# Optimization experiments

Measured on AMD Instinct MI355X. Metric: run time of the kernel, lower is better.

Reference implementation:

```python
import jax, jax.numpy as jnp
import numpy as np

T, B = 128, 64
STATE_DIM, LATENT_DIM, AC_DIM, MS_DIM = 32, 16, 8, 8
STATE_EMBED, AC_EMBED, HIDDEN, OUT_DIM = 64, 16, 64, 18


def setup_inputs() -> dict:
    key = jax.random.key(0)
    ks = jax.random.split(key, 18)
    f = lambda i, shape: jax.random.normal(ks[i], shape, jnp.float32)
    s = 0.05  # param scale
    return dict(
        state=f(0, (T, B, STATE_DIM)),
        latent_mean=f(1, (T, B, LATENT_DIM)),
        latent_logvar=f(2, (T, B, LATENT_DIM)) * 0.1,
        latent_mean_t=f(3, (T, B, LATENT_DIM)),
        latent_logvar_t=f(4, (T, B, LATENT_DIM)) * 0.1,
        agent_character=f(5, (T, B, AC_DIM)),
        mental_state=f(6, (T, B, MS_DIM)),
        partner_actions=jax.random.randint(ks[7], (T, B), 0, OUT_DIM, jnp.int32),
        dones=(jax.random.uniform(ks[8], (T, B)) < 0.05).astype(jnp.float32),
        W_state=f(9, (STATE_DIM, STATE_EMBED)) * s, b_state=jnp.zeros(STATE_EMBED),
        W_ac=f(10, (AC_DIM, AC_EMBED)) * s, b_ac=jnp.zeros(AC_EMBED),
        W_embed=f(11, (STATE_EMBED + AC_EMBED, HIDDEN)) * s, b_embed=jnp.zeros(HIDDEN),
        W_hid=f(12, (AC_EMBED + MS_DIM, HIDDEN)) * s, b_hid=jnp.zeros(HIDDEN),
        Wi=f(13, (HIDDEN, 3 * HIDDEN)) * s, bi=jnp.zeros(3 * HIDDEN),
        Wh_rz=f(14, (HIDDEN, 2 * HIDDEN)) * s,
        Wh_n=f(15, (HIDDEN, HIDDEN)) * s, bh_n=jnp.zeros(HIDDEN),
        W_out=f(16, (HIDDEN, OUT_DIM)) * s, b_out=jnp.zeros(OUT_DIM),
    )


def reference(state, latent_mean, latent_logvar, latent_mean_t, latent_logvar_t,
              agent_character, mental_state, partner_actions, dones,
              W_state, b_state, W_ac, b_ac, W_embed, b_embed, W_hid, b_hid,
              Wi, bi, Wh_rz, Wh_n, bh_n, W_out, b_out):
    Tn = state.shape[0]
    # ---- KL between consecutive latent Gaussians (with N(0,I) prior at t=0) ----
    lm = jnp.concatenate((latent_mean, latent_mean_t), -1)      # (T,B,2L)
    lv = jnp.concatenate((latent_logvar, latent_logvar_t), -1)
    G = lm.shape[-1]
    am = jnp.concatenate((jnp.zeros((1,) + lm.shape[1:], lm.dtype), lm))
    al = jnp.concatenate((jnp.zeros((1,) + lv.shape[1:], lv.dtype), lv))
    mu, m = am[1:], am[:-1]
    logE, logS = al[1:], al[:-1]
    kl = 0.5 * (logS.sum(-1) - logE.sum(-1) - G
                + jnp.exp(logE - logS).sum(-1)
                + ((m - mu) ** 2 / jnp.exp(logS)).sum(-1))      # (T,B)
    kl_loss = kl.sum()
    # ---- feature extractors ----
    se = jax.nn.relu(state @ W_state + b_state)                 # (T,B,SE)
    ae = jax.nn.relu(agent_character @ W_ac + b_ac)             # (T,B,AE)
    embed = jnp.concatenate((se, ae), -1) @ W_embed + b_embed   # (T,B,H)
    hidden = jnp.concatenate((ae, mental_state), -1) @ W_hid + b_hid  # (T,B,H)
    # ---- k-batch: K=T shifted trajectories, zero-padded at the tail ----
    idx = jnp.arange(Tn)[:, None] + jnp.arange(Tn)[None, :]     # (K,T)
    valid = idx < Tn                                            # (K,T) bool
    cidx = jnp.minimum(idx, Tn - 1)
    vf = valid.astype(embed.dtype)[..., None]                   # (K,T,1)
    k_embed = embed[cidx] * vf[..., None]                       # (K,T,B,H)
    k_hidden = hidden[cidx] * vf[..., None]                     # (K,T,B,H)
    k_dones = dones[cidx] * vf                                  # (K,T,B)
    k_actions = jnp.where(valid[..., None], partner_actions[cidx], 0)  # (K,T,B)
    # fill_to_first_true: 1 up to and including the first done of each k-traj
    episode_mask = (jnp.cumsum(k_dones, axis=1) - k_dones == 0).astype(embed.dtype)  # (K,T,B)
    # ---- GRU scan over timestep axis, vectorized over (K,B) ----
    h0 = k_hidden[:, 0]                                         # (K,B,H)
    xs = (jnp.moveaxis(k_embed, 1, 0), jnp.moveaxis(k_hidden, 1, 0), jnp.moveaxis(k_dones, 1, 0))

    def step(h, x):
        x_t, h0_t, d_t = x                                      # (K,B,H),(K,B,H),(K,B)
        h = jnp.where(d_t[..., None] > 0, h0_t, h)              # reset on done
        ir, iz, i_n = jnp.split(x_t @ Wi + bi, 3, -1)
        hr, hz = jnp.split(h @ Wh_rz, 2, -1)
        r = jax.nn.sigmoid(ir + hr)
        z = jax.nn.sigmoid(iz + hz)
        n = jnp.tanh(i_n + r * (h @ Wh_n + bh_n))
        h_new = (1.0 - z) * n + z * h
        return h_new, h_new

    _, hs = jax.lax.scan(step, h0, xs)                          # (T,K,B,H)
    logp = jax.nn.log_softmax(hs @ W_out + b_out, -1)           # (T,K,B,O)
    k_act_t = jnp.moveaxis(k_actions, 1, 0)                     # (T,K,B)
    nll = -jnp.take_along_axis(logp, k_act_t[..., None], -1)[..., 0]  # (T,K,B)
    mask = valid.T[:, :, None].astype(nll.dtype) * jnp.moveaxis(episode_mask, 1, 0)
    recon_loss = (nll * mask).sum(axis=1)                       # sum over K -> (T,B)
    return kl_loss, recon_loss
```

## Files before the change

### kernel.cpp

```cpp
#include <hip/hip_runtime.h>


#define XH_OFF   0
#define AUX_OFF  4194304
#define CTR_OFF  4227072

typedef float f32x16 __attribute__((ext_vector_type(16)));
typedef _Float16 h2 __attribute__((ext_vector_type(2)));

#if __has_builtin(__builtin_amdgcn_fdot2)
#define DOT2(a, b, c) __builtin_amdgcn_fdot2((a), (b), (c), false)
#else
#define DOT2(a, b, c) ((c) + (float)(a).x * (float)(b).x + (float)(a).y * (float)(b).y)
#endif

__device__ __forceinline__ h2 pack_pair(float h) {
  int hb = __builtin_bit_cast(int, h);
  int hp = __builtin_amdgcn_mov_dpp(hb, 0xB1, 0xF, 0xF, true);
  return __builtin_bit_cast(h2, __builtin_amdgcn_cvt_pkrtz(h, __builtin_bit_cast(float, hp)));
}

__device__ __forceinline__ float row16_scan_add(float v) {
  int t;
  t = __builtin_amdgcn_update_dpp(0, __builtin_bit_cast(int, v), 0x111, 0xF, 0xF, true);
  v += __builtin_bit_cast(float, t);
  t = __builtin_amdgcn_update_dpp(0, __builtin_bit_cast(int, v), 0x112, 0xF, 0xF, true);
  v += __builtin_bit_cast(float, t);
  t = __builtin_amdgcn_update_dpp(0, __builtin_bit_cast(int, v), 0x114, 0xF, 0xF, true);
  v += __builtin_bit_cast(float, t);
  t = __builtin_amdgcn_update_dpp(0, __builtin_bit_cast(int, v), 0x118, 0xF, 0xF, true);
  v += __builtin_bit_cast(float, t);
  return v;
}

__global__ __launch_bounds__(256, 1) void precompute_kernel(
    const float* __restrict__ state, const float* __restrict__ ac, const float* __restrict__ ms,
    const float* __restrict__ Wst, const float* __restrict__ bst,
    const float* __restrict__ Wac, const float* __restrict__ bac,
    const float* __restrict__ Wem, const float* __restrict__ bem,
    const float* __restrict__ Whd, const float* __restrict__ bhd,
    const float* __restrict__ Wi,  const float* __restrict__ bi,
    const float* __restrict__ lm, const float* __restrict__ lv,
    const float* __restrict__ lmt, const float* __restrict__ lvt,
    const float* __restrict__ dones, const int* __restrict__ actions,
    _Float16* __restrict__ xh, int* __restrict__ aux, float* __restrict__ out) {
  __shared__ float sWst[32 * 64];
  __shared__ float sWem[80 * 64];
  __shared__ float sWhd[24 * 64];
  __shared__ float sWac[8 * 16];
  __shared__ float sb[208];
  __shared__ float sin_[4][48];
  __shared__ float sse[4][80];
  __shared__ float semb[4][64];
  __shared__ float ps[4];
  int tid = threadIdx.x, lane = tid & 63, w = tid >> 6;

  if (blockIdx.x >= 256) {
    float total = 0.f;
    for (int it = 0; it < 16; ++it) {
      int idx = ((int)blockIdx.x - 256) * 256 + tid + it * 16384;
      int g = idx & 31;
      int pair = idx >> 5;
      const float* M = (g < 16) ? lm : lmt;
      const float* V = (g < 16) ? lv : lvt;
      int cur = pair * 16 + (g & 15);
      float mu = M[cur], lE = V[cur];
      float m = 0.f, lS = 0.f;
      if (pair >= 64) { m = M[cur - 1024]; lS = V[cur - 1024]; }
      float d = m - mu;
      total += 0.5f * (lS - lE - 1.f + __expf(lE - lS) + d * d * __expf(-lS));
    }
    #pragma unroll
    for (int off = 32; off; off >>= 1) total += __shfl_xor(total, off);
    if (lane == 0) ps[w] = total;
    __syncthreads();
    if (tid == 0) atomicAdd(out, ps[0] + ps[1] + ps[2] + ps[3]);
    return;
  }

  f32x16 wi0[4], wi1[4], wi2[4];
  #pragma unroll
  for (int k = 0; k < 64; ++k) {
    wi0[k >> 4][k & 15] = Wi[k * 192 + lane];
    wi1[k >> 4][k & 15] = Wi[k * 192 + 64 + lane];
    wi2[k >> 4][k & 15] = Wi[k * 192 + 128 + lane];
  }
  for (int i = tid; i < 32 * 64; i += 256) sWst[i] = Wst[i];
  for (int i = tid; i < 80 * 64; i += 256) sWem[i] = Wem[i];
  for (int i = tid; i < 24 * 64; i += 256) sWhd[i] = Whd[i];
  for (int i = tid; i < 8 * 16; i += 256) sWac[i] = Wac[i];
  if (tid < 64) sb[tid] = bst[tid];
  if (tid < 16) sb[64 + tid] = bac[tid];
  if (tid < 64) sb[80 + tid] = bem[tid];
  if (tid < 64) sb[144 + tid] = bhd[tid];
  float bi0 = bi[lane], bi1 = bi[64 + lane], bi2 = bi[128 + lane];
  __syncthreads();
  for (int cnt = 0; cnt < 8; ++cnt) {
    int pair = blockIdx.x * 32 + w * 8 + cnt;
    if (lane < 32)      sin_[w][lane] = state[pair * 32 + lane];
    else if (lane < 40) sin_[w][lane] = ac[pair * 8 + (lane - 32)];
    else if (lane < 48) sin_[w][lane] = ms[pair * 8 + (lane - 40)];
    if (lane == 0) aux[pair] = (dones[pair] > 0.f ? (int)0x80000000 : 0) | actions[pair];
    __syncthreads();
    float se = sb[lane];
    #pragma unroll
    for (int k = 0; k < 32; ++k) se += sin_[w][k] * sWst[k * 64 + lane];
    se = fmaxf(se, 0.f);
    float ae = 0.f;
    if (lane < 16) {
      ae = sb[64 + lane];
      #pragma unroll
      for (int k = 0; k < 8; ++k) ae += sin_[w][32 + k] * sWac[k * 16 + lane];
      ae = fmaxf(ae, 0.f);
    }
    __syncthreads();
    sse[w][lane] = se;
    if (lane < 16) sse[w][64 + lane] = ae;
    __syncthreads();
    float em = sb[80 + lane];
    #pragma unroll
    for (int k = 0; k < 80; ++k) em += sse[w][k] * sWem[k * 64 + lane];
    float hd = sb[144 + lane];
    #pragma unroll
    for (int k = 0; k < 16; ++k) hd += sse[w][64 + k] * sWhd[k * 64 + lane];
    #pragma unroll
    for (int k = 0; k < 8; ++k) hd += sin_[w][40 + k] * sWhd[(16 + k) * 64 + lane];
    semb[w][lane] = em;
    __syncthreads();
    float x0 = bi0, x1 = bi1, x2 = bi2;
    #pragma unroll
    for (int k = 0; k < 64; ++k) {
      float e = semb[w][k];
      x0 += e * wi0[k >> 4][k & 15];
      x1 += e * wi1[k >> 4][k & 15];
      x2 += e * wi2[k >> 4][k & 15];
    }
    _Float16* xo = xh + pair * 256;
    xo[lane] = (_Float16)x0; xo[64 + lane] = (_Float16)x1;
    xo[128 + lane] = (_Float16)x2; xo[192 + lane] = (_Float16)hd;
    __syncthreads();
  }
}

__global__ __launch_bounds__(64, 2) void rollout_kernel(
    const _Float16* __restrict__ xh, const int* __restrict__ aux,
    const float* __restrict__ Whrz, const float* __restrict__ Whn,
    const float* __restrict__ bhn, const float* __restrict__ Wout,
    const float* __restrict__ bout, float* __restrict__ out,
    unsigned int* __restrict__ ctrs) {
  __shared__ __attribute__((aligned(16))) h2 sh2[32];
  int lane = threadIdx.x;
  int row = (lane < 18) ? lane : 0;
  h2 Wr[32], Wz[32], Wn[32], Wo[32];
  #pragma unroll
  for (int k = 0; k < 32; ++k) {
    Wr[k] = h2{(_Float16)Whrz[(2 * k) * 128 + lane],      (_Float16)Whrz[(2 * k + 1) * 128 + lane]};
    Wz[k] = h2{(_Float16)Whrz[(2 * k) * 128 + 64 + lane], (_Float16)Whrz[(2 * k + 1) * 128 + 64 + lane]};
    Wn[k] = h2{(_Float16)Whn[(2 * k) * 64 + lane],        (_Float16)Whn[(2 * k + 1) * 64 + lane]};
    Wo[k] = h2{(_Float16)Wout[(2 * k) * 18 + row],        (_Float16)Wout[(2 * k + 1) * 18 + row]};
  }
  float bhn_r = bhn[lane];
  float bo_r = bout[row];
  __syncthreads();
  const uint4* shv = (const uint4*)sh2;
  int q = blockIdx.x & 7;
  while (true) {
    int i = 0;
    if (lane == 0) i = (int)atomicAdd(&ctrs[q], 1u);
    i = __shfl(i, 0);
    if (i >= 1024) break;
    int t = i >> 3, b = ((i & 7) << 3) | q;
    int u = t;
    int pr = (t << 6) | b;
    const _Float16* xb = xh + pr * 256;
    float h = (float)xb[192 + lane];
    float x0 = (float)xb[lane], x1 = (float)xb[64 + lane], x2 = (float)xb[128 + lane];
    int ax = aux[pr];
    if ((lane & 1) == 0) sh2[lane >> 1] = pack_pair(h);
    for (int s = 0;; ++s) {
      int un = (u < 127) ? u + 1 : 127;
      int prn = (un << 6) | b;
      const _Float16* xn = xh + prn * 256;
      float nx0 = (float)xn[lane], nx1 = (float)xn[64 + lane], nx2 = (float)xn[128 + lane];
      float nh = (float)xn[192 + lane];
      int nax = aux[prn];
      float ara = x0, arb = 0.f, aza = x1, azb = 0.f, ana = 0.f, anb = 0.f;
      #pragma unroll
      for (int qq = 0; qq < 8; ++qq) {
        uint4 hv = shv[qq];
        h2 a0 = __builtin_bit_cast(h2, hv.x);
        h2 a1 = __builtin_bit_cast(h2, hv.y);
        h2 a2 = __builtin_bit_cast(h2, hv.z);
        h2 a3 = __builtin_bit_cast(h2, hv.w);
        ara = DOT2(a0, Wr[4 * qq + 0], ara); arb = DOT2(a1, Wr[4 * qq + 1], arb);
        ara = DOT2(a2, Wr[4 * qq + 2], ara); arb = DOT2(a3, Wr[4 * qq + 3], arb);
        aza = DOT2(a0, Wz[4 * qq + 0], aza); azb = DOT2(a1, Wz[4 * qq + 1], azb);
        aza = DOT2(a2, Wz[4 * qq + 2], aza); azb = DOT2(a3, Wz[4 * qq + 3], azb);
        ana = DOT2(a0, Wn[4 * qq + 0], ana); anb = DOT2(a1, Wn[4 * qq + 1], anb);
        ana = DOT2(a2, Wn[4 * qq + 2], ana); anb = DOT2(a3, Wn[4 * qq + 3], anb);
      }
      float ar = ara + arb, az = aza + azb, an = ana + anb;
      float r = __builtin_amdgcn_rcpf(1.f + __expf(-ar));
      float z = __builtin_amdgcn_rcpf(1.f + __expf(-az));
      float pre = x2 + r * (an + bhn_r);
      float n = 1.f - 2.f * __builtin_amdgcn_rcpf(1.f + __expf(2.f * pre));
      float hn = (1.f - z) * n + z * h;
      if ((lane & 1) == 0) sh2[lane >> 1] = pack_pair(hn);
      float la_a = bo_r, la_b = 0.f;
      #pragma unroll
      for (int qq = 0; qq < 8; ++qq) {
        uint4 hv = shv[qq];
        la_a = DOT2(__builtin_bit_cast(h2, hv.x), Wo[4 * qq + 0], la_a);
        la_b = DOT2(__builtin_bit_cast(h2, hv.y), Wo[4 * qq + 1], la_b);
        la_a = DOT2(__builtin_bit_cast(h2, hv.z), Wo[4 * qq + 2], la_a);
        la_b = DOT2(__builtin_bit_cast(h2, hv.w), Wo[4 * qq + 3], la_b);
      }
      float logit = la_a + la_b;
      float e = (lane < 18) ? __expf(logit) : 0.f;
      float er = row16_scan_add(e);
      float ssum = __builtin_bit_cast(float, __builtin_amdgcn_readlane(__builtin_bit_cast(int, er), 15))
                 + __builtin_bit_cast(float, __builtin_amdgcn_readlane(__builtin_bit_cast(int, er), 31));
      int act = ax & 0xFFFF;
      float la = __builtin_bit_cast(float, __builtin_amdgcn_readlane(__builtin_bit_cast(int, logit), act));
      float lse = __logf(ssum);
      if (lane == 0) atomicAdd(&out[1 + s * 64 + b], lse - la);
      if (ax < 0 || u == 127) break;
      u = un; x0 = nx0; x1 = nx1; x2 = nx2; ax = nax;
      if (nax < 0) {
        h = nh;
        if ((lane & 1) == 0) sh2[lane >> 1] = pack_pair(h);
      } else {
        h = hn;
      }
    }
  }
}

extern "C" void kernel_launch(void* const* d_in, const int* in_sizes, int n_in,
                              void* d_out, int out_size, void* d_ws, size_t ws_size,
                              hipStream_t stream) {
  const float* state = (const float*)d_in[0];
  const float* lm    = (const float*)d_in[1];
  const float* lv    = (const float*)d_in[2];
  const float* lmt   = (const float*)d_in[3];
  const float* lvt   = (const float*)d_in[4];
  const float* ac    = (const float*)d_in[5];
  const float* ms    = (const float*)d_in[6];
  const int*   actions = (const int*)d_in[7];
  const float* dones = (const float*)d_in[8];
  const float* Wst = (const float*)d_in[9],  *bst = (const float*)d_in[10];
  const float* Wac = (const float*)d_in[11], *bac = (const float*)d_in[12];
  const float* Wem = (const float*)d_in[13], *bem = (const float*)d_in[14];
  const float* Whd = (const float*)d_in[15], *bhd = (const float*)d_in[16];
  const float* Wi  = (const float*)d_in[17], *bi  = (const float*)d_in[18];
  const float* Whrz = (const float*)d_in[19];
  const float* Whn  = (const float*)d_in[20], *bhn = (const float*)d_in[21];
  const float* Wout = (const float*)d_in[22], *bout = (const float*)d_in[23];
  float* out = (float*)d_out;
  _Float16* xh = (_Float16*)((char*)d_ws + XH_OFF);
  int* aux = (int*)((char*)d_ws + AUX_OFF);
  unsigned int* ctrs = (unsigned int*)((char*)d_ws + CTR_OFF);

  hipMemsetAsync(d_out, 0, (size_t)out_size * sizeof(float), stream);
  hipMemsetAsync(ctrs, 0, 8 * sizeof(unsigned int), stream);

  hipLaunchKernelGGL(precompute_kernel, dim3(320), dim3(256), 0, stream,
                     state, ac, ms, Wst, bst, Wac, bac, Wem, bem, Whd, bhd, Wi, bi,
                     lm, lv, lmt, lvt, dones, actions, xh, aux, out);
  hipLaunchKernelGGL(rollout_kernel, dim3(2048), dim3(64), 0, stream,
                     xh, aux, Whrz, Whn, bhn, Wout, bout, out, ctrs);
}
```

Baseline: 186.1 us.

## Process two rollout start times per wavefront with packed fp16 math

```diff
diff --git a/kernel.cpp b/kernel.cpp
--- a/kernel.cpp
+++ b/kernel.cpp
@@ -8,17 +8,8 @@
 typedef float f32x16 __attribute__((ext_vector_type(16)));
 typedef _Float16 h2 __attribute__((ext_vector_type(2)));
 
-#if __has_builtin(__builtin_amdgcn_fdot2)
-#define DOT2(a, b, c) __builtin_amdgcn_fdot2((a), (b), (c), false)
-#else
-#define DOT2(a, b, c) ((c) + (float)(a).x * (float)(b).x + (float)(a).y * (float)(b).y)
-#endif
-
-__device__ __forceinline__ h2 pack_pair(float h) {
-  int hb = __builtin_bit_cast(int, h);
-  int hp = __builtin_amdgcn_mov_dpp(hb, 0xB1, 0xF, 0xF, true);
-  return __builtin_bit_cast(h2, __builtin_amdgcn_cvt_pkrtz(h, __builtin_bit_cast(float, hp)));
-}
+__device__ __forceinline__ h2 sp0(h2 v) { return __builtin_shufflevector(v, v, 0, 0); }
+__device__ __forceinline__ h2 sp1(h2 v) { return __builtin_shufflevector(v, v, 1, 1); }
 
 __device__ __forceinline__ float row16_scan_add(float v) {
   int t;
@@ -31,6 +22,10 @@
   t = __builtin_amdgcn_update_dpp(0, __builtin_bit_cast(int, v), 0x118, 0xF, 0xF, true);
   v += __builtin_bit_cast(float, t);
   return v;
+}
+
+__device__ __forceinline__ float rl(float v, int l) {
+  return __builtin_bit_cast(float, __builtin_amdgcn_readlane(__builtin_bit_cast(int, v), l));
 }
 
 __global__ __launch_bounds__(256, 1) void precompute_kernel(
@@ -142,13 +137,13 @@
   }
 }
 
-__global__ __launch_bounds__(64, 2) void rollout_kernel(
+__global__ __launch_bounds__(64, 1) void rollout_kernel(
     const _Float16* __restrict__ xh, const int* __restrict__ aux,
     const float* __restrict__ Whrz, const float* __restrict__ Whn,
     const float* __restrict__ bhn, const float* __restrict__ Wout,
     const float* __restrict__ bout, float* __restrict__ out,
     unsigned int* __restrict__ ctrs) {
-  __shared__ __attribute__((aligned(16))) h2 sh2[32];
+  __shared__ __attribute__((aligned(16))) h2 shab[64];
   int lane = threadIdx.x;
   int row = (lane < 18) ? lane : 0;
   h2 Wr[32], Wz[32], Wn[32], Wo[32];
@@ -162,76 +157,100 @@
   float bhn_r = bhn[lane];
   float bo_r = bout[row];
   __syncthreads();
-  const uint4* shv = (const uint4*)sh2;
+  const uint4* shv = (const uint4*)shab;
   int q = blockIdx.x & 7;
   while (true) {
     int i = 0;
     if (lane == 0) i = (int)atomicAdd(&ctrs[q], 1u);
     i = __shfl(i, 0);
-    if (i >= 1024) break;
-    int t = i >> 3, b = ((i & 7) << 3) | q;
-    int u = t;
-    int pr = (t << 6) | b;
+    if (i >= 512) break;
+    int tp = i >> 3, b = ((i & 7) << 3) | q;
+    int tA = tp << 1, tB = tA | 1;
+    int u = tA;
+    int pr = (u << 6) | b;
     const _Float16* xb = xh + pr * 256;
-    float h = (float)xb[192 + lane];
     float x0 = (float)xb[lane], x1 = (float)xb[64 + lane], x2 = (float)xb[128 + lane];
+    float h0u = (float)xb[192 + lane];
     int ax = aux[pr];
-    if ((lane & 1) == 0) sh2[lane >> 1] = pack_pair(h);
-    for (int s = 0;; ++s) {
+    float hA = h0u, hB = h0u;
+    bool okA = true;
+    shab[lane] = __builtin_bit_cast(h2, __builtin_amdgcn_cvt_pkrtz(hA, hB));
+    for (;;) {
       int un = (u < 127) ? u + 1 : 127;
       int prn = (un << 6) | b;
       const _Float16* xn = xh + prn * 256;
       float nx0 = (float)xn[lane], nx1 = (float)xn[64 + lane], nx2 = (float)xn[128 + lane];
-      float nh = (float)xn[192 + lane];
+      float nh0 = (float)xn[192 + lane];
       int nax = aux[prn];
-      float ara = x0, arb = 0.f, aza = x1, azb = 0.f, ana = 0.f, anb = 0.f;
+      h2 ra = {(_Float16)0.f, (_Float16)0.f}, rb = ra, za = ra, zb = ra, na_ = ra, nb_ = ra;
       #pragma unroll
-      for (int qq = 0; qq < 8; ++qq) {
-        uint4 hv = shv[qq];
-        h2 a0 = __builtin_bit_cast(h2, hv.x);
-        h2 a1 = __builtin_bit_cast(h2, hv.y);
-        h2 a2 = __builtin_bit_cast(h2, hv.z);
-        h2 a3 = __builtin_bit_cast(h2, hv.w);
-        ara = DOT2(a0, Wr[4 * qq + 0], ara); arb = DOT2(a1, Wr[4 * qq + 1], arb);
-        ara = DOT2(a2, Wr[4 * qq + 2], ara); arb = DOT2(a3, Wr[4 * qq + 3], arb);
-        aza = DOT2(a0, Wz[4 * qq + 0], aza); azb = DOT2(a1, Wz[4 * qq + 1], azb);
-        aza = DOT2(a2, Wz[4 * qq + 2], aza); azb = DOT2(a3, Wz[4 * qq + 3], azb);
-        ana = DOT2(a0, Wn[4 * qq + 0], ana); anb = DOT2(a1, Wn[4 * qq + 1], anb);
-        ana = DOT2(a2, Wn[4 * qq + 2], ana); anb = DOT2(a3, Wn[4 * qq + 3], anb);
+      for (int m = 0; m < 16; ++m) {
+        uint4 hv = shv[m];
+        h2 p0 = __builtin_bit_cast(h2, hv.x);
+        h2 p1 = __builtin_bit_cast(h2, hv.y);
+        h2 p2 = __builtin_bit_cast(h2, hv.z);
+        h2 p3 = __builtin_bit_cast(h2, hv.w);
+        h2 wr0 = Wr[2 * m], wr1 = Wr[2 * m + 1];
+        h2 wz0 = Wz[2 * m], wz1 = Wz[2 * m + 1];
+        h2 wn0 = Wn[2 * m], wn1 = Wn[2 * m + 1];
+        ra += p0 * sp0(wr0); rb += p1 * sp1(wr0);
+        ra += p2 * sp0(wr1); rb += p3 * sp1(wr1);
+        za += p0 * sp0(wz0); zb += p1 * sp1(wz0);
+        za += p2 * sp0(wz1); zb += p3 * sp1(wz1);
+        na_ += p0 * sp0(wn0); nb_ += p1 * sp1(wn0);
+        na_ += p2 * sp0(wn1); nb_ += p3 * sp1(wn1);
       }
-      float ar = ara + arb, az = aza + azb, an = ana + anb;
-      float r = __builtin_amdgcn_rcpf(1.f + __expf(-ar));
-      float z = __builtin_amdgcn_rcpf(1.f + __expf(-az));
-      float pre = x2 + r * (an + bhn_r);
-      float n = 1.f - 2.f * __builtin_amdgcn_rcpf(1.f + __expf(2.f * pre));
-      float hn = (1.f - z) * n + z * h;
-      if ((lane & 1) == 0) sh2[lane >> 1] = pack_pair(hn);
-      float la_a = bo_r, la_b = 0.f;
+      float arA = x0 + (float)ra[0] + (float)rb[0];
+      float arB = x0 + (float)ra[1] + (float)rb[1];
+      float azA = x1 + (float)za[0] + (float)zb[0];
+      float azB = x1 + (float)za[1] + (float)zb[1];
+      float anA = bhn_r + (float)na_[0] + (float)nb_[0];
+      float anB = bhn_r + (float)na_[1] + (float)nb_[1];
+      float rrA = __builtin_amdgcn_rcpf(1.f + __expf(-arA));
+      float rrB = __builtin_amdgcn_rcpf(1.f + __expf(-arB));
+      float zzA = __builtin_amdgcn_rcpf(1.f + __expf(-azA));
+      float zzB = __builtin_amdgcn_rcpf(1.f + __expf(-azB));
+      float preA = x2 + rrA * anA;
+      float preB = x2 + rrB * anB;
+      float nnA = 1.f - 2.f * __builtin_amdgcn_rcpf(1.f + __expf(2.f * preA));
+      float nnB = 1.f - 2.f * __builtin_amdgcn_rcpf(1.f + __expf(2.f * preB));
+      float hnA = (1.f - zzA) * nnA + zzA * hA;
+      float hnB = (1.f - zzB) * nnB + zzB * hB;
+      shab[lane] = __builtin_bit_cast(h2, __builtin_amdgcn_cvt_pkrtz(hnA, hnB));
+      h2 la = {(_Float16)0.f, (_Float16)0.f}, lb = la;
       #pragma unroll
-      for (int qq = 0; qq < 8; ++qq) {
-        uint4 hv = shv[qq];
-        la_a = DOT2(__builtin_bit_cast(h2, hv.x), Wo[4 * qq + 0], la_a);
-        la_b = DOT2(__builtin_bit_cast(h2, hv.y), Wo[4 * qq + 1], la_b);
-        la_a = DOT2(__builtin_bit_cast(h2, hv.z), Wo[4 * qq + 2], la_a);
-        la_b = DOT2(__builtin_bit_cast(h2, hv.w), Wo[4 * qq + 3], la_b);
+      for (int m = 0; m < 16; ++m) {
+        uint4 hv = shv[m];
+        h2 wo0 = Wo[2 * m], wo1 = Wo[2 * m + 1];
+        la += __builtin_bit_cast(h2, hv.x) * sp0(wo0);
+        lb += __builtin_bit_cast(h2, hv.y) * sp1(wo0);
+        la += __builtin_bit_cast(h2, hv.z) * sp0(wo1);
+        lb += __builtin_bit_cast(h2, hv.w) * sp1(wo1);
       }
-      float logit = la_a + la_b;
-      float e = (lane < 18) ? __expf(logit) : 0.f;
-      float er = row16_scan_add(e);
-      float ssum = __builtin_bit_cast(float, __builtin_amdgcn_readlane(__builtin_bit_cast(int, er), 15))
-                 + __builtin_bit_cast(float, __builtin_amdgcn_readlane(__builtin_bit_cast(int, er), 31));
+      float lgA = bo_r + (float)la[0] + (float)lb[0];
+      float lgB = bo_r + (float)la[1] + (float)lb[1];
+      float eA = (lane < 18) ? __expf(lgA) : 0.f;
+      float eB = (lane < 18) ? __expf(lgB) : 0.f;
+      float sA = row16_scan_add(eA);
+      float sB = row16_scan_add(eB);
+      float ssA = rl(sA, 15) + rl(sA, 31);
+      float ssB = rl(sB, 15) + rl(sB, 31);
       int act = ax & 0xFFFF;
-      float la = __builtin_bit_cast(float, __builtin_amdgcn_readlane(__builtin_bit_cast(int, logit), act));
-      float lse = __logf(ssum);
-      if (lane == 0) atomicAdd(&out[1 + s * 64 + b], lse - la);
-      if (ax < 0 || u == 127) break;
-      u = un; x0 = nx0; x1 = nx1; x2 = nx2; ax = nax;
-      if (nax < 0) {
-        h = nh;
-        if ((lane & 1) == 0) sh2[lane >> 1] = pack_pair(h);
-      } else {
-        h = hn;
+      float laA = rl(lgA, act);
+      float laB = rl(lgB, act);
+      if (lane == 0) {
+        if (okA)     atomicAdd(&out[1 + (u - tA) * 64 + b], __logf(ssA) - laA);
+        if (u >= tB) atomicAdd(&out[1 + (u - tB) * 64 + b], __logf(ssB) - laB);
       }
+      bool dpos = ax < 0;
+      if ((dpos && u >= tB) || u == 127) break;
+      if (dpos) okA = false;
+      u = un; x0 = nx0; x1 = nx1; x2 = nx2; ax = nax; h0u = nh0;
+      bool rstA = (ax < 0);
+      bool rstB = rstA || (u == tB);
+      hA = rstA ? h0u : hnA;
+      hB = rstB ? h0u : hnB;
+      shab[lane] = __builtin_bit_cast(h2, __builtin_amdgcn_cvt_pkrtz(hA, hB));
     }
   }
 }
```

Result: slower. 289.6 us (+55.6%).
